# Optimization experiments

Hardware: AMD Instinct MI355X
Metric: run time of the kernel (lower is better)

Reference implementation:

```python
import jax, jax.numpy as jnp
import numpy as np
from jax import lax

BETA = 0.5
ITERATIONS = 20
EPS = 1e-12


def setup_inputs() -> dict:
    key = jax.random.key(0)
    n, K = 32768, 512
    # C plays the role of a cosine-similarity matrix; randn keeps exp(C/beta) bounded.
    C = jax.random.normal(key, (n, K), dtype=jnp.float32)
    return {"C": C}


def reference(C):
    n, K = C.shape
    a = jnp.float32(1.0 / n)          # uniform row marginal (scalar broadcast of a = ones(n,1)/n)
    b = jnp.float32(1.0 / K)          # uniform column marginal
    K_mat = jnp.exp(C / BETA)         # [n, K]
    Q0 = jnp.full((n, K), 1.0 / (n * K), dtype=C.dtype)
    sigma0 = jnp.full((K,), 1.0 / K, dtype=C.dtype)

    def step(carry, _):
        Q, sigma = carry
        Q = K_mat * sigma[None, :]                              # elementwise column scaling
        Q = Q / (jnp.sum(Q, axis=1, keepdims=True) + EPS) * a   # row-normalize to marginal a
        sigma = b / (jnp.sum(Q, axis=0) + EPS)                  # column sums (== Q^T @ ones)
        return (Q, sigma), None

    (Q, sigma), _ = lax.scan(step, (Q0, sigma0), None, length=ITERATIONS)
    return Q * n
```

## Files before the change

kernel.cpp:

```cpp
#include <hip/hip_runtime.h>
#include <cmath>


namespace {
constexpr int ROWS = 32768;
constexpr int COLS = 512;
constexpr int ITERS = 20;
constexpr float EPS = 1e-12f;
constexpr float A_M = 1.0f / 32768.0f;
constexpr float B_M = 1.0f / 512.0f;
constexpr float L2E2 = 2.8853900817779268f;
constexpr int WPB = 4;
constexpr int NSH = 8;
constexpr int SLAB_ROWS = ROWS / 8;
constexpr int GSIG_OFF = 0;
constexpr int TSUM_OFF = ITERS * COLS;
constexpr size_t CTRL_FLOATS = (size_t)TSUM_OFF + (size_t)(ITERS - 1) * NSH * COLS;
constexpr size_t KB_BYTES = (size_t)ROWS * COLS * 2;
constexpr int MID_BLOCKS = 1024;
constexpr int MID_RPW = 8;
constexpr int BIG_BLOCKS = 2048;
constexpr int BIG_RPW = 4;

typedef float f4v __attribute__((ext_vector_type(4)));
}

__device__ __forceinline__ float bflo(unsigned u) {
  union { unsigned i; float f; } v; v.i = u << 16; return v.f;
}
__device__ __forceinline__ float bfhi(unsigned u) {
  union { unsigned i; float f; } v; v.i = u & 0xFFFF0000u; return v.f;
}
__device__ __forceinline__ unsigned f2bf(float f) {
  union { float f; unsigned u; } v; v.f = f;
  return (v.u + 0x7FFFu + ((v.u >> 16) & 1u)) >> 16;
}
__device__ __forceinline__ int row_base_mid(int bid, int wave) {
  return (bid & 7) * SLAB_ROWS + ((bid >> 3) * WPB + wave) * MID_RPW;
}
__device__ __forceinline__ int row_base_big(int bid, int wave) {
  return (bid & 7) * SLAB_ROWS + ((bid >> 3) * WPB + wave) * BIG_RPW;
}

__global__ __launch_bounds__(256) void ipot_zero_kernel(float* __restrict__ ctrl) {
  const size_t stride = (size_t)gridDim.x * blockDim.x;
  const size_t gtid = (size_t)blockIdx.x * blockDim.x + threadIdx.x;
  if (gtid < COLS) ctrl[GSIG_OFF + gtid] = B_M;
  const size_t tsz = (size_t)(ITERS - 1) * NSH * COLS;
  for (size_t i = gtid; i < tsz; i += stride) ctrl[TSUM_OFF + i] = 0.0f;
}

template <bool NT_C>
__global__ __launch_bounds__(256, 8) void ipot_pass0_kernel(
    const float* __restrict__ C, unsigned short* __restrict__ Kb,
    float* __restrict__ ctrl) {
  __shared__ float part[WPB][COLS];
  const int tid = threadIdx.x;
  const int wave = tid >> 6;
  const int lane = tid & 63;
  const int wrow = row_base_big(blockIdx.x, wave);

  f4v c0[BIG_RPW], c1[BIG_RPW];
#pragma unroll
  for (int r = 0; r < BIG_RPW; ++r) {
    const f4v* rp = (const f4v*)(C + (size_t)(wrow + r) * COLS);
    if (NT_C) {
      c0[r] = __builtin_nontemporal_load(&rp[2 * lane]);
      c1[r] = __builtin_nontemporal_load(&rp[2 * lane + 1]);
    } else {
      c0[r] = rp[2 * lane];
      c1[r] = rp[2 * lane + 1];
    }
  }

  float p[BIG_RPW];
#pragma unroll
  for (int r = 0; r < BIG_RPW; ++r) {
    c0[r].x = exp2f(c0[r].x * L2E2); c0[r].y = exp2f(c0[r].y * L2E2);
    c0[r].z = exp2f(c0[r].z * L2E2); c0[r].w = exp2f(c0[r].w * L2E2);
    c1[r].x = exp2f(c1[r].x * L2E2); c1[r].y = exp2f(c1[r].y * L2E2);
    c1[r].z = exp2f(c1[r].z * L2E2); c1[r].w = exp2f(c1[r].w * L2E2);
    uint4 kp;
    kp.x = f2bf(c0[r].x) | (f2bf(c0[r].y) << 16);
    kp.y = f2bf(c0[r].z) | (f2bf(c0[r].w) << 16);
    kp.z = f2bf(c1[r].x) | (f2bf(c1[r].y) << 16);
    kp.w = f2bf(c1[r].z) | (f2bf(c1[r].w) << 16);
    ((uint4*)(Kb + (size_t)(wrow + r) * COLS))[lane] = kp;
    p[r] = ((c0[r].x + c0[r].y) + (c0[r].z + c0[r].w)) +
           ((c1[r].x + c1[r].y) + (c1[r].z + c1[r].w));
  }
#pragma unroll
  for (int off = 32; off; off >>= 1) {
#pragma unroll
    for (int r = 0; r < BIG_RPW; ++r) p[r] += __shfl_xor(p[r], off, 64);
  }
  float a[8] = {0.f, 0.f, 0.f, 0.f, 0.f, 0.f, 0.f, 0.f};
#pragma unroll
  for (int r = 0; r < BIG_RPW; ++r) {
    const float inv = 1.0f / (B_M * p[r] + EPS);
    a[0] += c0[r].x * inv; a[1] += c0[r].y * inv;
    a[2] += c0[r].z * inv; a[3] += c0[r].w * inv;
    a[4] += c1[r].x * inv; a[5] += c1[r].y * inv;
    a[6] += c1[r].z * inv; a[7] += c1[r].w * inv;
  }
  *(float4*)&part[wave][8 * lane] = *(float4*)&a[0];
  *(float4*)&part[wave][8 * lane + 4] = *(float4*)&a[4];
  __syncthreads();
  float* ts = ctrl + TSUM_OFF + (size_t)(blockIdx.x & 7) * COLS;
  int j = tid;
  atomicAdd(&ts[j], part[0][j] + part[1][j] + part[2][j] + part[3][j]);
  j += 256;
  atomicAdd(&ts[j], part[0][j] + part[1][j] + part[2][j] + part[3][j]);
}

__global__ __launch_bounds__(256, 4) void ipot_mid_kernel(
    const unsigned short* __restrict__ Kb, float* __restrict__ ctrl, int t) {
  __shared__ float sig[COLS];
  __shared__ float part[WPB][COLS];
  const int tid = threadIdx.x;
  const int wave = tid >> 6;
  const int lane = tid & 63;
  const int wrow = row_base_mid(blockIdx.x, wave);

  const float* gsp = ctrl + GSIG_OFF + (size_t)(t - 1) * COLS;
  const float* tb = ctrl + TSUM_OFF + (size_t)(t - 1) * NSH * COLS;
  float tv0[NSH], tv1[NSH];
#pragma unroll
  for (int s = 0; s < NSH; ++s) {
    tv0[s] = tb[s * COLS + tid];
    tv1[s] = tb[s * COLS + tid + 256];
  }
  const float g0 = gsp[tid];
  const float g1 = gsp[tid + 256];

  uint4 kr[MID_RPW];
#pragma unroll
  for (int r = 0; r < MID_RPW; ++r)
    kr[r] = ((const uint4*)(Kb + (size_t)(wrow + r) * COLS))[lane];

  {
    float T0 = 0.f, T1 = 0.f;
#pragma unroll
    for (int s = 0; s < NSH; ++s) { T0 += tv0[s]; T1 += tv1[s]; }
    const float sv0 = B_M / (g0 * A_M * T0 + EPS);
    const float sv1 = B_M / (g1 * A_M * T1 + EPS);
    sig[tid] = sv0;
    sig[tid + 256] = sv1;
    if (blockIdx.x == 0) {
      float* gsc = ctrl + GSIG_OFF + (size_t)t * COLS;
      gsc[tid] = sv0;
      gsc[tid + 256] = sv1;
    }
  }
  __syncthreads();

  const float4 sA = *(const float4*)&sig[8 * lane];
  const float4 sB = *(const float4*)&sig[8 * lane + 4];

  float p[MID_RPW];
#pragma unroll
  for (int r = 0; r < MID_RPW; ++r) {
    p[r] = bflo(kr[r].x) * sA.x + bfhi(kr[r].x) * sA.y +
           bflo(kr[r].y) * sA.z + bfhi(kr[r].y) * sA.w +
           bflo(kr[r].z) * sB.x + bfhi(kr[r].z) * sB.y +
           bflo(kr[r].w) * sB.z + bfhi(kr[r].w) * sB.w;
  }
#pragma unroll
  for (int off = 32; off; off >>= 1) {
#pragma unroll
    for (int r = 0; r < MID_RPW; ++r) p[r] += __shfl_xor(p[r], off, 64);
  }
  float a[8] = {0.f, 0.f, 0.f, 0.f, 0.f, 0.f, 0.f, 0.f};
#pragma unroll
  for (int r = 0; r < MID_RPW; ++r) {
    const float inv = 1.0f / (p[r] + EPS);
    a[0] += bflo(kr[r].x) * inv; a[1] += bfhi(kr[r].x) * inv;
    a[2] += bflo(kr[r].y) * inv; a[3] += bfhi(kr[r].y) * inv;
    a[4] += bflo(kr[r].z) * inv; a[5] += bfhi(kr[r].z) * inv;
    a[6] += bflo(kr[r].w) * inv; a[7] += bfhi(kr[r].w) * inv;
  }
  *(float4*)&part[wave][8 * lane] = *(float4*)&a[0];
  *(float4*)&part[wave][8 * lane + 4] = *(float4*)&a[4];
  __syncthreads();
  float* ts = ctrl + TSUM_OFF +
              ((size_t)t * NSH + (blockIdx.x & 7)) * COLS;
  int j = tid;
  atomicAdd(&ts[j], part[0][j] + part[1][j] + part[2][j] + part[3][j]);
  j += 256;
  atomicAdd(&ts[j], part[0][j] + part[1][j] + part[2][j] + part[3][j]);
}

__global__ __launch_bounds__(256, 8) void ipot_final_kb_kernel(
    const unsigned short* __restrict__ Kb, float* __restrict__ out,
    const float* __restrict__ ctrl) {
  __shared__ float sig[COLS];
  const int tid = threadIdx.x;
  const int wave = tid >> 6;
  const int lane = tid & 63;
  const int wrow = row_base_big(blockIdx.x, wave);

  const int t = ITERS - 1;
  const float* gsp = ctrl + GSIG_OFF + (size_t)(t - 1) * COLS;
  const float* tb = ctrl + TSUM_OFF + (size_t)(t - 1) * NSH * COLS;
  float tv0[NSH], tv1[NSH];
#pragma unroll
  for (int s = 0; s < NSH; ++s) {
    tv0[s] = tb[s * COLS + tid];
    tv1[s] = tb[s * COLS + tid + 256];
  }
  const float g0 = gsp[tid];
  const float g1 = gsp[tid + 256];

  uint4 kr[BIG_RPW];
#pragma unroll
  for (int r = 0; r < BIG_RPW; ++r)
    kr[r] = ((const uint4*)(Kb + (size_t)(wrow + r) * COLS))[lane];

  {
    float T0 = 0.f, T1 = 0.f;
#pragma unroll
    for (int s = 0; s < NSH; ++s) { T0 += tv0[s]; T1 += tv1[s]; }
    sig[tid] = B_M / (g0 * A_M * T0 + EPS);
    sig[tid + 256] = B_M / (g1 * A_M * T1 + EPS);
  }
  __syncthreads();

  const float4 sA = *(const float4*)&sig[8 * lane];
  const float4 sB = *(const float4*)&sig[8 * lane + 4];

  float p[BIG_RPW];
#pragma unroll
  for (int r = 0; r < BIG_RPW; ++r) {
    p[r] = bflo(kr[r].x) * sA.x + bfhi(kr[r].x) * sA.y +
           bflo(kr[r].y) * sA.z + bfhi(kr[r].y) * sA.w +
           bflo(kr[r].z) * sB.x + bfhi(kr[r].z) * sB.y +
           bflo(kr[r].w) * sB.z + bfhi(kr[r].w) * sB.w;
  }
#pragma unroll
  for (int off = 32; off; off >>= 1) {
#pragma unroll
    for (int r = 0; r < BIG_RPW; ++r) p[r] += __shfl_xor(p[r], off, 64);
  }
#pragma unroll
  for (int r = 0; r < BIG_RPW; ++r) {
    const float inv = 1.0f / (p[r] + EPS);
    f4v* wp = (f4v*)(out + (size_t)(wrow + r) * COLS);
    f4v o0, o1;
    o0.x = bflo(kr[r].x) * sA.x * inv; o0.y = bfhi(kr[r].x) * sA.y * inv;
    o0.z = bflo(kr[r].y) * sA.z * inv; o0.w = bfhi(kr[r].y) * sA.w * inv;
    o1.x = bflo(kr[r].z) * sB.x * inv; o1.y = bfhi(kr[r].z) * sB.y * inv;
    o1.z = bflo(kr[r].w) * sB.z * inv; o1.w = bfhi(kr[r].w) * sB.w * inv;
    __builtin_nontemporal_store(o0, &wp[2 * lane]);
    __builtin_nontemporal_store(o1, &wp[2 * lane + 1]);
  }
}

__global__ __launch_bounds__(256, 8) void ipot_final_c_kernel(
    const float* __restrict__ C, float* __restrict__ out,
    const float* __restrict__ ctrl) {
  __shared__ float sig[COLS];
  const int tid = threadIdx.x;
  const int wave = tid >> 6;
  const int lane = tid & 63;
  const int wrow = row_base_big(blockIdx.x, wave);

  const int t = ITERS - 1;
  const float* gsp = ctrl + GSIG_OFF + (size_t)(t - 1) * COLS;
  const float* tb = ctrl + TSUM_OFF + (size_t)(t - 1) * NSH * COLS;
  float tv0[NSH], tv1[NSH];
#pragma unroll
  for (int s = 0; s < NSH; ++s) {
    tv0[s] = tb[s * COLS + tid];
    tv1[s] = tb[s * COLS + tid + 256];
  }
  const float g0 = gsp[tid];
  const float g1 = gsp[tid + 256];

  f4v c0[BIG_RPW], c1[BIG_RPW];
#pragma unroll
  for (int r = 0; r < BIG_RPW; ++r) {
    const f4v* rp = (const f4v*)(C + (size_t)(wrow + r) * COLS);
    c0[r] = rp[2 * lane];
    c1[r] = rp[2 * lane + 1];
  }
  {
    float T0 = 0.f, T1 = 0.f;
#pragma unroll
    for (int s = 0; s < NSH; ++s) { T0 += tv0[s]; T1 += tv1[s]; }
    sig[tid] = B_M / (g0 * A_M * T0 + EPS);
    sig[tid + 256] = B_M / (g1 * A_M * T1 + EPS);
  }
  __syncthreads();

  const float4 sA = *(const float4*)&sig[8 * lane];
  const float4 sB = *(const float4*)&sig[8 * lane + 4];

  float p[BIG_RPW];
#pragma unroll
  for (int r = 0; r < BIG_RPW; ++r) {
    c0[r].x = exp2f(c0[r].x * L2E2); c0[r].y = exp2f(c0[r].y * L2E2);
    c0[r].z = exp2f(c0[r].z * L2E2); c0[r].w = exp2f(c0[r].w * L2E2);
    c1[r].x = exp2f(c1[r].x * L2E2); c1[r].y = exp2f(c1[r].y * L2E2);
    c1[r].z = exp2f(c1[r].z * L2E2); c1[r].w = exp2f(c1[r].w * L2E2);
    p[r] = c0[r].x * sA.x + c0[r].y * sA.y + c0[r].z * sA.z + c0[r].w * sA.w +
           c1[r].x * sB.x + c1[r].y * sB.y + c1[r].z * sB.z + c1[r].w * sB.w;
  }
#pragma unroll
  for (int off = 32; off; off >>= 1) {
#pragma unroll
    for (int r = 0; r < BIG_RPW; ++r) p[r] += __shfl_xor(p[r], off, 64);
  }
#pragma unroll
  for (int r = 0; r < BIG_RPW; ++r) {
    const float inv = 1.0f / (p[r] + EPS);
    f4v* wp = (f4v*)(out + (size_t)(wrow + r) * COLS);
    f4v o0, o1;
    o0.x = c0[r].x * sA.x * inv; o0.y = c0[r].y * sA.y * inv;
    o0.z = c0[r].z * sA.z * inv; o0.w = c0[r].w * sA.w * inv;
    o1.x = c1[r].x * sB.x * inv; o1.y = c1[r].y * sB.y * inv;
    o1.z = c1[r].z * sB.z * inv; o1.w = c1[r].w * sB.w * inv;
    __builtin_nontemporal_store(o0, &wp[2 * lane]);
    __builtin_nontemporal_store(o1, &wp[2 * lane + 1]);
  }
}

extern "C" void kernel_launch(void* const* d_in, const int* in_sizes, int n_in,
                              void* d_out, int out_size, void* d_ws, size_t ws_size,
                              hipStream_t stream) {
  const float* C = (const float*)d_in[0];
  float* out = (float*)d_out;

  const bool kb_in_ws = ws_size >= KB_BYTES + CTRL_FLOATS * sizeof(float);
  unsigned short* Kb;
  float* ctrl;
  if (kb_in_ws) {
    Kb = (unsigned short*)d_ws;
    ctrl = (float*)((char*)d_ws + KB_BYTES);
  } else {
    Kb = (unsigned short*)(out + (size_t)ROWS * COLS / 2);
    ctrl = (float*)d_ws;
  }

  ipot_zero_kernel<<<128, 256, 0, stream>>>(ctrl);
  if (kb_in_ws)
    ipot_pass0_kernel<true><<<BIG_BLOCKS, 256, 0, stream>>>(C, Kb, ctrl);
  else
    ipot_pass0_kernel<false><<<BIG_BLOCKS, 256, 0, stream>>>(C, Kb, ctrl);
  for (int t = 1; t < ITERS - 1; ++t)
    ipot_mid_kernel<<<MID_BLOCKS, 256, 0, stream>>>(Kb, ctrl, t);
  if (kb_in_ws)
    ipot_final_kb_kernel<<<BIG_BLOCKS, 256, 0, stream>>>(Kb, out, ctrl);
  else
    ipot_final_c_kernel<<<BIG_BLOCKS, 256, 0, stream>>>(C, out, ctrl);
}
```

Before: 185.0 us.

## Replace per-iteration kernel launches with a persistent cooperative kernel using grid barriers

Adds a single persistent cooperative kernel that loads C once, keeps the bf16 exp(C/beta) tile in registers for all iterations, and synchronises column sums across blocks with atomic counters acting as a grid barrier. This removes about 20 kernel launches and the repeated re-reading of the bf16 K matrix from global memory each iteration. It falls back to the multi-kernel path if occupancy or cooperative launch fails. It risks barrier spin overhead, register pressure at the lower occupancy bound, and the fallback path no longer supports the case where the K matrix cannot fit in the workspace.

```diff
diff --git a/kernel.cpp b/kernel.cpp
--- a/kernel.cpp
+++ b/kernel.cpp
@@ -10,13 +10,17 @@
 constexpr float A_M = 1.0f / 32768.0f;
 constexpr float B_M = 1.0f / 512.0f;
 constexpr float L2E2 = 2.8853900817779268f;
-constexpr int WPB = 4;
 constexpr int NSH = 8;
 constexpr int SLAB_ROWS = ROWS / 8;
 constexpr int GSIG_OFF = 0;
 constexpr int TSUM_OFF = ITERS * COLS;
-constexpr size_t CTRL_FLOATS = (size_t)TSUM_OFF + (size_t)(ITERS - 1) * NSH * COLS;
+constexpr int CNT_OFF = TSUM_OFF + (ITERS - 1) * NSH * COLS;
+constexpr int CNT_UINTS = ((ITERS - 1) * 8 + (ITERS - 1)) * 16;
 constexpr size_t KB_BYTES = (size_t)ROWS * COLS * 2;
+constexpr size_t CTRL_FLOATS = (size_t)CNT_OFF + CNT_UINTS;
+constexpr int PBLK = 1024;
+constexpr int PRPW = 8;
+constexpr int WPB = 4;
 constexpr int MID_BLOCKS = 1024;
 constexpr int MID_RPW = 8;
 constexpr int BIG_BLOCKS = 2048;
@@ -46,8 +50,143 @@
   const size_t stride = (size_t)gridDim.x * blockDim.x;
   const size_t gtid = (size_t)blockIdx.x * blockDim.x + threadIdx.x;
   if (gtid < COLS) ctrl[GSIG_OFF + gtid] = B_M;
-  const size_t tsz = (size_t)(ITERS - 1) * NSH * COLS;
-  for (size_t i = gtid; i < tsz; i += stride) ctrl[TSUM_OFF + i] = 0.0f;
+  const size_t zsz = (size_t)(ITERS - 1) * NSH * COLS + CNT_UINTS;
+  for (size_t i = gtid; i < zsz; i += stride) ctrl[TSUM_OFF + i] = 0.0f;
+}
+
+__global__ __launch_bounds__(256, 4) void ipot_persist_kernel(
+    const float* __restrict__ C, float* __restrict__ out,
+    float* __restrict__ ctrl) {
+  __shared__ float sig[COLS];
+  __shared__ float part[4][COLS];
+  const int tid = threadIdx.x;
+  const int wave = tid >> 6;
+  const int lane = tid & 63;
+  const int slab = blockIdx.x & 7;
+  const int gw = blockIdx.x * 4 + wave;
+  const size_t row0 = (size_t)gw * PRPW;
+  unsigned* cnt = (unsigned*)(ctrl + CNT_OFF);
+
+  unsigned kb[PRPW][4];
+  {
+    const float* rp = C + row0 * COLS + 8 * lane;
+    f4v c0 = __builtin_nontemporal_load((const f4v*)rp);
+    f4v c1 = __builtin_nontemporal_load((const f4v*)(rp + 4));
+#pragma unroll
+    for (int r = 0; r < PRPW; ++r) {
+      f4v d0 = c0, d1 = c1;
+      if (r + 1 < PRPW) {
+        const float* np = rp + (size_t)(r + 1) * COLS;
+        c0 = __builtin_nontemporal_load((const f4v*)np);
+        c1 = __builtin_nontemporal_load((const f4v*)(np + 4));
+      }
+      d0.x = exp2f(d0.x * L2E2); d0.y = exp2f(d0.y * L2E2);
+      d0.z = exp2f(d0.z * L2E2); d0.w = exp2f(d0.w * L2E2);
+      d1.x = exp2f(d1.x * L2E2); d1.y = exp2f(d1.y * L2E2);
+      d1.z = exp2f(d1.z * L2E2); d1.w = exp2f(d1.w * L2E2);
+      kb[r][0] = f2bf(d0.x) | (f2bf(d0.y) << 16);
+      kb[r][1] = f2bf(d0.z) | (f2bf(d0.w) << 16);
+      kb[r][2] = f2bf(d1.x) | (f2bf(d1.y) << 16);
+      kb[r][3] = f2bf(d1.z) | (f2bf(d1.w) << 16);
+    }
+  }
+  sig[tid] = B_M;
+  sig[tid + 256] = B_M;
+  __syncthreads();
+
+  for (int t = 0; t < ITERS - 1; ++t) {
+    const float4 sA = *(const float4*)&sig[8 * lane];
+    const float4 sB = *(const float4*)&sig[8 * lane + 4];
+    float p[PRPW];
+#pragma unroll
+    for (int r = 0; r < PRPW; ++r) {
+      p[r] = bflo(kb[r][0]) * sA.x + bfhi(kb[r][0]) * sA.y +
+             bflo(kb[r][1]) * sA.z + bfhi(kb[r][1]) * sA.w +
+             bflo(kb[r][2]) * sB.x + bfhi(kb[r][2]) * sB.y +
+             bflo(kb[r][3]) * sB.z + bfhi(kb[r][3]) * sB.w;
+    }
+#pragma unroll
+    for (int off = 32; off; off >>= 1) {
+#pragma unroll
+      for (int r = 0; r < PRPW; ++r) p[r] += __shfl_xor(p[r], off, 64);
+    }
+    float a[8] = {0.f, 0.f, 0.f, 0.f, 0.f, 0.f, 0.f, 0.f};
+#pragma unroll
+    for (int r = 0; r < PRPW; ++r) {
+      const float inv = 1.0f / (p[r] + EPS);
+      a[0] += bflo(kb[r][0]) * inv; a[1] += bfhi(kb[r][0]) * inv;
+      a[2] += bflo(kb[r][1]) * inv; a[3] += bfhi(kb[r][1]) * inv;
+      a[4] += bflo(kb[r][2]) * inv; a[5] += bfhi(kb[r][2]) * inv;
+      a[6] += bflo(kb[r][3]) * inv; a[7] += bfhi(kb[r][3]) * inv;
+    }
+    *(float4*)&part[wave][8 * lane] = *(float4*)&a[0];
+    *(float4*)&part[wave][8 * lane + 4] = *(float4*)&a[4];
+    __syncthreads();
+    float* ts = ctrl + TSUM_OFF + ((size_t)t * NSH + slab) * COLS;
+    atomicAdd(&ts[tid],
+              part[0][tid] + part[1][tid] + part[2][tid] + part[3][tid]);
+    atomicAdd(&ts[tid + 256], part[0][tid + 256] + part[1][tid + 256] +
+                                  part[2][tid + 256] + part[3][tid + 256]);
+
+    __syncthreads();
+    if (tid == 0) {
+      unsigned* sc = cnt + (t * 8 + slab) * 16;
+      unsigned* gc = cnt + ((ITERS - 1) * 8 + t) * 16;
+      unsigned prev = __hip_atomic_fetch_add(sc, 1u, __ATOMIC_RELAXED,
+                                             __HIP_MEMORY_SCOPE_AGENT);
+      if (prev == (PBLK / 8 - 1))
+        __hip_atomic_fetch_add(gc, 1u, __ATOMIC_RELAXED,
+                               __HIP_MEMORY_SCOPE_AGENT);
+      while (__hip_atomic_load(gc, __ATOMIC_RELAXED,
+                               __HIP_MEMORY_SCOPE_AGENT) < 8u)
+        __builtin_amdgcn_s_sleep(2);
+    }
+    __syncthreads();
+    __builtin_amdgcn_fence(__ATOMIC_ACQUIRE, "agent");
+
+    float* tb = ctrl + TSUM_OFF + (size_t)t * NSH * COLS;
+    float T0 = 0.f, T1 = 0.f;
+#pragma unroll
+    for (int s = 0; s < NSH; ++s) {
+      T0 += __hip_atomic_load(&tb[s * COLS + tid], __ATOMIC_RELAXED,
+                              __HIP_MEMORY_SCOPE_AGENT);
+      T1 += __hip_atomic_load(&tb[s * COLS + tid + 256], __ATOMIC_RELAXED,
+                              __HIP_MEMORY_SCOPE_AGENT);
+    }
+    sig[tid] = B_M / (sig[tid] * A_M * T0 + EPS);
+    sig[tid + 256] = B_M / (sig[tid + 256] * A_M * T1 + EPS);
+    __syncthreads();
+  }
+
+  {
+    const float4 sA = *(const float4*)&sig[8 * lane];
+    const float4 sB = *(const float4*)&sig[8 * lane + 4];
+    float p[PRPW];
+#pragma unroll
+    for (int r = 0; r < PRPW; ++r) {
+      p[r] = bflo(kb[r][0]) * sA.x + bfhi(kb[r][0]) * sA.y +
+             bflo(kb[r][1]) * sA.z + bfhi(kb[r][1]) * sA.w +
+             bflo(kb[r][2]) * sB.x + bfhi(kb[r][2]) * sB.y +
+             bflo(kb[r][3]) * sB.z + bfhi(kb[r][3]) * sB.w;
+    }
+#pragma unroll
+    for (int off = 32; off; off >>= 1) {
+#pragma unroll
+      for (int r = 0; r < PRPW; ++r) p[r] += __shfl_xor(p[r], off, 64);
+    }
+#pragma unroll
+    for (int r = 0; r < PRPW; ++r) {
+      const float inv = 1.0f / (p[r] + EPS);
+      float* wp = out + (row0 + r) * COLS + 8 * lane;
+      f4v o0, o1;
+      o0.x = bflo(kb[r][0]) * sA.x * inv; o0.y = bfhi(kb[r][0]) * sA.y * inv;
+      o0.z = bflo(kb[r][1]) * sA.z * inv; o0.w = bfhi(kb[r][1]) * sA.w * inv;
+      o1.x = bflo(kb[r][2]) * sB.x * inv; o1.y = bfhi(kb[r][2]) * sB.y * inv;
+      o1.z = bflo(kb[r][3]) * sB.z * inv; o1.w = bfhi(kb[r][3]) * sB.w * inv;
+      __builtin_nontemporal_store(o0, (f4v*)wp);
+      __builtin_nontemporal_store(o1, (f4v*)(wp + 4));
+    }
+  }
 }
 
 template <bool NT_C>
@@ -72,7 +211,6 @@
       c1[r] = rp[2 * lane + 1];
     }
   }
-
   float p[BIG_RPW];
 #pragma unroll
   for (int r = 0; r < BIG_RPW; ++r) {
@@ -137,7 +275,6 @@
 #pragma unroll
   for (int r = 0; r < MID_RPW; ++r)
     kr[r] = ((const uint4*)(Kb + (size_t)(wrow + r) * COLS))[lane];
-
   {
     float T0 = 0.f, T1 = 0.f;
 #pragma unroll
@@ -156,7 +293,6 @@
 
   const float4 sA = *(const float4*)&sig[8 * lane];
   const float4 sB = *(const float4*)&sig[8 * lane + 4];
-
   float p[MID_RPW];
 #pragma unroll
   for (int r = 0; r < MID_RPW; ++r) {
@@ -182,8 +318,7 @@
   *(float4*)&part[wave][8 * lane] = *(float4*)&a[0];
   *(float4*)&part[wave][8 * lane + 4] = *(float4*)&a[4];
   __syncthreads();
-  float* ts = ctrl + TSUM_OFF +
-              ((size_t)t * NSH + (blockIdx.x & 7)) * COLS;
+  float* ts = ctrl + TSUM_OFF + ((size_t)t * NSH + (blockIdx.x & 7)) * COLS;
   int j = tid;
   atomicAdd(&ts[j], part[0][j] + part[1][j] + part[2][j] + part[3][j]);
   j += 256;
@@ -215,7 +350,6 @@
 #pragma unroll
   for (int r = 0; r < BIG_RPW; ++r)
     kr[r] = ((const uint4*)(Kb + (size_t)(wrow + r) * COLS))[lane];
-
   {
     float T0 = 0.f, T1 = 0.f;
 #pragma unroll
@@ -227,7 +361,6 @@
 
   const float4 sA = *(const float4*)&sig[8 * lane];
   const float4 sB = *(const float4*)&sig[8 * lane + 4];
-
   float p[BIG_RPW];
 #pragma unroll
   for (int r = 0; r < BIG_RPW; ++r) {
@@ -255,101 +388,33 @@
   }
 }
 
-__global__ __launch_bounds__(256, 8) void ipot_final_c_kernel(
-    const float* __restrict__ C, float* __restrict__ out,
-    const float* __restrict__ ctrl) {
-  __shared__ float sig[COLS];
-  const int tid = threadIdx.x;
-  const int wave = tid >> 6;
-  const int lane = tid & 63;
-  const int wrow = row_base_big(blockIdx.x, wave);
-
-  const int t = ITERS - 1;
-  const float* gsp = ctrl + GSIG_OFF + (size_t)(t - 1) * COLS;
-  const float* tb = ctrl + TSUM_OFF + (size_t)(t - 1) * NSH * COLS;
-  float tv0[NSH], tv1[NSH];
-#pragma unroll
-  for (int s = 0; s < NSH; ++s) {
-    tv0[s] = tb[s * COLS + tid];
-    tv1[s] = tb[s * COLS + tid + 256];
-  }
-  const float g0 = gsp[tid];
-  const float g1 = gsp[tid + 256];
-
-  f4v c0[BIG_RPW], c1[BIG_RPW];
-#pragma unroll
-  for (int r = 0; r < BIG_RPW; ++r) {
-    const f4v* rp = (const f4v*)(C + (size_t)(wrow + r) * COLS);
-    c0[r] = rp[2 * lane];
-    c1[r] = rp[2 * lane + 1];
-  }
-  {
-    float T0 = 0.f, T1 = 0.f;
-#pragma unroll
-    for (int s = 0; s < NSH; ++s) { T0 += tv0[s]; T1 += tv1[s]; }
-    sig[tid] = B_M / (g0 * A_M * T0 + EPS);
-    sig[tid + 256] = B_M / (g1 * A_M * T1 + EPS);
-  }
-  __syncthreads();
-
-  const float4 sA = *(const float4*)&sig[8 * lane];
-  const float4 sB = *(const float4*)&sig[8 * lane + 4];
-
-  float p[BIG_RPW];
-#pragma unroll
-  for (int r = 0; r < BIG_RPW; ++r) {
-    c0[r].x = exp2f(c0[r].x * L2E2); c0[r].y = exp2f(c0[r].y * L2E2);
-    c0[r].z = exp2f(c0[r].z * L2E2); c0[r].w = exp2f(c0[r].w * L2E2);
-    c1[r].x = exp2f(c1[r].x * L2E2); c1[r].y = exp2f(c1[r].y * L2E2);
-    c1[r].z = exp2f(c1[r].z * L2E2); c1[r].w = exp2f(c1[r].w * L2E2);
-    p[r] = c0[r].x * sA.x + c0[r].y * sA.y + c0[r].z * sA.z + c0[r].w * sA.w +
-           c1[r].x * sB.x + c1[r].y * sB.y + c1[r].z * sB.z + c1[r].w * sB.w;
-  }
-#pragma unroll
-  for (int off = 32; off; off >>= 1) {
-#pragma unroll
-    for (int r = 0; r < BIG_RPW; ++r) p[r] += __shfl_xor(p[r], off, 64);
-  }
-#pragma unroll
-  for (int r = 0; r < BIG_RPW; ++r) {
-    const float inv = 1.0f / (p[r] + EPS);
-    f4v* wp = (f4v*)(out + (size_t)(wrow + r) * COLS);
-    f4v o0, o1;
-    o0.x = c0[r].x * sA.x * inv; o0.y = c0[r].y * sA.y * inv;
-    o0.z = c0[r].z * sA.z * inv; o0.w = c0[r].w * sA.w * inv;
-    o1.x = c1[r].x * sB.x * inv; o1.y = c1[r].y * sB.y * inv;
-    o1.z = c1[r].z * sB.z * inv; o1.w = c1[r].w * sB.w * inv;
-    __builtin_nontemporal_store(o0, &wp[2 * lane]);
-    __builtin_nontemporal_store(o1, &wp[2 * lane + 1]);
-  }
-}
-
 extern "C" void kernel_launch(void* const* d_in, const int* in_sizes, int n_in,
                               void* d_out, int out_size, void* d_ws, size_t ws_size,
                               hipStream_t stream) {
   const float* C = (const float*)d_in[0];
   float* out = (float*)d_out;
-
-  const bool kb_in_ws = ws_size >= KB_BYTES + CTRL_FLOATS * sizeof(float);
-  unsigned short* Kb;
-  float* ctrl;
-  if (kb_in_ws) {
-    Kb = (unsigned short*)d_ws;
-    ctrl = (float*)((char*)d_ws + KB_BYTES);
-  } else {
-    Kb = (unsigned short*)(out + (size_t)ROWS * COLS / 2);
-    ctrl = (float*)d_ws;
-  }
+  unsigned short* Kb = (unsigned short*)d_ws;
+  float* ctrl = (float*)((char*)d_ws + KB_BYTES);
+  const bool ws_ok = ws_size >= KB_BYTES + CTRL_FLOATS * sizeof(float);
+  if (!ws_ok) ctrl = (float*)d_ws;
 
   ipot_zero_kernel<<<128, 256, 0, stream>>>(ctrl);
-  if (kb_in_ws)
+
+  int occ = 0;
+  hipError_t oe = hipOccupancyMaxActiveBlocksPerMultiprocessor(
+      &occ, reinterpret_cast<const void*>(&ipot_persist_kernel), 256, 0);
+  bool persist = ws_ok && (oe == hipSuccess) && (occ >= 4);
+  if (persist) {
+    void* args[] = {(void*)&C, (void*)&out, (void*)&ctrl};
+    hipError_t ce = hipLaunchCooperativeKernel(
+        reinterpret_cast<void*>(&ipot_persist_kernel), dim3(PBLK), dim3(256),
+        args, 0, stream);
+    if (ce != hipSuccess) persist = false;
+  }
+  if (!persist) {
     ipot_pass0_kernel<true><<<BIG_BLOCKS, 256, 0, stream>>>(C, Kb, ctrl);
-  else
-    ipot_pass0_kernel<false><<<BIG_BLOCKS, 256, 0, stream>>>(C, Kb, ctrl);
-  for (int t = 1; t < ITERS - 1; ++t)
-    ipot_mid_kernel<<<MID_BLOCKS, 256, 0, stream>>>(Kb, ctrl, t);
-  if (kb_in_ws)
+    for (int t = 1; t < ITERS - 1; ++t)
+      ipot_mid_kernel<<<MID_BLOCKS, 256, 0, stream>>>(Kb, ctrl, t);
     ipot_final_kb_kernel<<<BIG_BLOCKS, 256, 0, stream>>>(Kb, out, ctrl);
-  else
-    ipot_final_c_kernel<<<BIG_BLOCKS, 256, 0, stream>>>(C, out, ctrl);
-}
+  }
+}
```

After: 182.2 us. No clear change (-1.5%).
